# Optimization experiments

Measured on AMD Instinct MI355X. Metric: run time of the kernel, lower is better.

## Reference

```python
import jax, jax.numpy as jnp
import numpy as np

N = 100000
E = 1600000
H = 2          # attention heads
C = 64         # hidden_dim (per-head out channels)
VOCAB = 501    # attr_dims[0] + 1
NUM_GRAPHS = 512
NEG_SLOPE = 0.2


def gat_conv(h_in, src, dst, W, a_src, a_dst, bias):
    # h_in: [N, Fin]; W: [Fin, H*C]; a_src/a_dst: [H, C]; bias: [H*C]
    h = (h_in @ W).reshape(N, H, C)                      # [N,H,C]
    alpha_s = jnp.sum(h * a_src[None], axis=-1)          # [N,H]
    alpha_d = jnp.sum(h * a_dst[None], axis=-1)          # [N,H]
    e = jax.nn.leaky_relu(alpha_s[src] + alpha_d[dst], NEG_SLOPE)  # [Etot,H]
    # segment softmax over incoming edges of each dst node
    m = jax.ops.segment_max(e, dst, num_segments=N)      # [N,H]
    ex = jnp.exp(e - m[dst])
    s = jax.ops.segment_sum(ex, dst, num_segments=N)     # [N,H]
    alpha = ex / (s[dst] + 1e-16)                        # [Etot,H]
    out = jax.ops.segment_sum(h[src] * alpha[:, :, None], dst, num_segments=N)
    return out.reshape(N, H * C) + bias


def layer_norm(x, g, b):
    mu = jnp.mean(x, axis=-1, keepdims=True)
    var = jnp.var(x, axis=-1, keepdims=True)
    return (x - mu) / jnp.sqrt(var + 1e-5) * g + b


def setup_inputs() -> dict:
    key = jax.random.key(0)
    ks = jax.random.split(key, 16)
    x = jax.random.randint(ks[0], (N, 1), 0, 500, dtype=jnp.int64)
    edge_index = jax.random.randint(ks[1], (2, E), 0, N, dtype=jnp.int64)
    batch_idx = jnp.sort(jax.random.randint(ks[2], (N,), 0, NUM_GRAPHS, dtype=jnp.int64))
    sc = 0.1
    return {
        "x": x, "edge_index": edge_index, "batch_idx": batch_idx,
        "emb": jax.random.normal(ks[3], (VOCAB, C), jnp.float32) * sc,
        "W1": jax.random.normal(ks[4], (C, H * C), jnp.float32) * sc,
        "a_src1": jax.random.normal(ks[5], (H, C), jnp.float32) * sc,
        "a_dst1": jax.random.normal(ks[6], (H, C), jnp.float32) * sc,
        "b1": jnp.zeros((H * C,), jnp.float32),
        "ln_g": jnp.ones((H * C,), jnp.float32),
        "ln_b": jnp.zeros((H * C,), jnp.float32),
        "W2": jax.random.normal(ks[7], (H * C, H * C), jnp.float32) * sc,
        "a_src2": jax.random.normal(ks[8], (H, C), jnp.float32) * sc,
        "a_dst2": jax.random.normal(ks[9], (H, C), jnp.float32) * sc,
        "b2": jnp.zeros((H * C,), jnp.float32),
        "Wp": jax.random.normal(ks[10], (H * C, C), jnp.float32) * sc,
        "bp": jnp.zeros((C,), jnp.float32),
    }


def reference(x, edge_index, batch_idx, emb, W1, a_src1, a_dst1, b1, ln_g, ln_b, W2, a_src2, a_dst2, b2, Wp, bp):
    # add self-loops (PyG GATConv default add_self_loops=True)
    loops = jnp.arange(N, dtype=edge_index.dtype)
    src = jnp.concatenate([edge_index[0], loops])
    dst = jnp.concatenate([edge_index[1], loops])

    x_emb = emb[x[:, 0]]                                  # [N,C] (embedding + squeeze(1))
    h = gat_conv(x_emb, src, dst, W1, a_src1, a_dst1, b1)  # [N,2C]
    h = jax.nn.gelu(layer_norm(h, ln_g, ln_b), approximate=False)  # dropout off (eval)
    h = gat_conv(h, src, dst, W2, a_src2, a_dst2, b2)      # [N,2C]
    h = h @ Wp + bp                                        # [N,C]
    # global mean pool over graphs
    ssum = jax.ops.segment_sum(h, batch_idx, num_segments=NUM_GRAPHS)
    cnt = jax.ops.segment_sum(jnp.ones((N,), h.dtype), batch_idx, num_segments=NUM_GRAPHS)
    z = ssum / jnp.maximum(cnt, 1.0)[:, None]
    return h, z
```

## Files before the change

kernel.cpp:

```cpp
#include <hip/hip_runtime.h>
#include <hip/hip_bf16.h>
#include <math.h>

#define H2C 128
#define CDIM 64
#define CAP 48

typedef short s16x8 __attribute__((ext_vector_type(8)));
typedef unsigned short u16x8 __attribute__((ext_vector_type(8)));
typedef float f32x4 __attribute__((ext_vector_type(4)));

static __device__ __forceinline__ float wred64(float x) {
#pragma unroll
  for (int off = 32; off; off >>= 1) x += __shfl_xor(x, off, 64);
  return x;
}
static __device__ __forceinline__ ushort f2bfu(float x) {
  __hip_bfloat16 b = __float2bfloat16(x);
  return *reinterpret_cast<ushort*>(&b);
}
static __device__ __forceinline__ float bfu2f(ushort u) {
  unsigned int x = ((unsigned int)u) << 16;
  return __int_as_float((int)x);
}
static __device__ __forceinline__ float erf_fast(float x) {
  float ax = fabsf(x);
  float t = __fdividef(1.f, 1.f + 0.3275911f * ax);
  float y = t * (0.254829592f + t * (-0.284496736f +
            t * (1.421413741f + t * (-1.453152027f + t * 1.061405429f))));
  float e = 1.f - y * __expf(-ax * ax);
  return copysignf(e, x);
}

__global__ void k_embw(const float* __restrict__ emb, const float* __restrict__ W1,
                       const float* __restrict__ a_src, const float* __restrict__ a_dst,
                       float* __restrict__ embW, float* __restrict__ asv, float* __restrict__ adv)
{
  int v = blockIdx.x;
  int j = threadIdx.x;
  const float* er = emb + v * CDIM;
  float acc = 0.f;
#pragma unroll
  for (int k = 0; k < CDIM; ++k) acc += er[k] * W1[k * H2C + j];
  embW[v * H2C + j] = acc;
  float ps = wred64(acc * a_src[j]);
  float pd = wred64(acc * a_dst[j]);
  if ((j & 63) == 0) {
    int h = j >> 6;
    asv[v * 2 + h] = ps;
    adv[v * 2 + h] = pd;
  }
}

__global__ void k_w2prep(const float* __restrict__ W2,
                         const float* __restrict__ as2w, const float* __restrict__ ad2w,
                         ushort* __restrict__ w2bt, float* __restrict__ was, float* __restrict__ wad)
{
  int k = blockIdx.x;
  int c = threadIdx.x;
  float w = W2[k * H2C + c];
  w2bt[c * H2C + k] = f2bfu(w);
  int h = c >> 6;
  float s = wred64(w * as2w[c]);
  float d = wred64(w * ad2w[c]);
  if ((c & 63) == 0) { was[k * 2 + h] = s; wad[k * 2 + h] = d; }
}

__global__ void k_wpprep(const float* __restrict__ Wp, ushort* __restrict__ wpbt)
{
  int k = blockIdx.x;
  int c = threadIdx.x;
  wpbt[c * H2C + k] = f2bfu(Wp[k * CDIM + c]);
}

__global__ void __launch_bounds__(256)
k_scatter(const int* __restrict__ ei, const int* __restrict__ xv,
          int* __restrict__ count, unsigned* __restrict__ col4,
          int E, int N, int chunk)
{
  int xcd = blockIdx.x & 7;
  int ig  = blockIdx.x >> 3;
  int nb  = gridDim.x >> 3;
  int lo = xcd * chunk;
  int hi = lo + chunk; if (hi > N) hi = N;
  int stride = nb * 256;
  for (int e = ig * 256 + threadIdx.x; e < E; e += stride) {
    int d = ei[E + e];
    if (d < lo || d >= hi) continue;
    int s = ei[e];
    int slot = atomicAdd(&count[d], 1);
    if (slot < CAP)
      col4[(size_t)d * CAP + slot] = (unsigned)s | ((unsigned)xv[s] << 17);
  }
}

__global__ void __launch_bounds__(256)
k_gath1(const int* __restrict__ count, const unsigned* __restrict__ col4,
        const int* __restrict__ xv,
        const float2* __restrict__ asv, const float2* __restrict__ adv,
        const float* __restrict__ embW,
        const float* __restrict__ b1, const float* __restrict__ lng,
        const float* __restrict__ lnb,
        const float* __restrict__ was, const float* __restrict__ wad,
        ushort* __restrict__ g, float2* __restrict__ as2,
        float2* __restrict__ ad2, int N)
{
  int lane = threadIdx.x & 63;
  int wv = (blockIdx.x * blockDim.x + threadIdx.x) >> 6;
  int nw = (gridDim.x * blockDim.x) >> 6;
  int grp = lane >> 4, l16 = lane & 15;
  int headL = l16 >> 3;
  int cb = l16 * 8;
  float b1c[8], lngc[8], lnbc[8], was0[8], was1[8], wad0[8], wad1[8];
#pragma unroll
  for (int j = 0; j < 8; ++j) {
    b1c[j] = b1[cb + j]; lngc[j] = lng[cb + j]; lnbc[j] = lnb[cb + j];
    was0[j] = was[(cb + j) * 2]; was1[j] = was[(cb + j) * 2 + 1];
    wad0[j] = wad[(cb + j) * 2]; wad1[j] = wad[(cb + j) * 2 + 1];
  }
  for (int base = wv * 4; base < N; base += nw * 4) {
    int r = base + grp;
    bool valid = r < N;
    int cnt = 0, vd = 0;
    float adh = 0.f;
    if (valid) {
      cnt = count[r]; if (cnt > CAP) cnt = CAP;
      vd = xv[r];
      float2 ad = adv[vd];
      adh = headL ? ad.y : ad.x;
    }
    size_t rb = (size_t)r * CAP;
    float acc[8] = {0.f, 0.f, 0.f, 0.f, 0.f, 0.f, 0.f, 0.f};
    float s = 0.f;
    auto proc = [&](int vi) {
      float2 a_ = asv[vi];
      float e = (headL ? a_.y : a_.x) + adh; e = e >= 0.f ? e : 0.2f * e;
      float ex = __expf(e);
      s += ex;
      const float4* vp = (const float4*)&embW[(size_t)vi * H2C + cb];
      float4 va = vp[0], vb = vp[1];
      acc[0] += ex * va.x; acc[1] += ex * va.y;
      acc[2] += ex * va.z; acc[3] += ex * va.w;
      acc[4] += ex * vb.x; acc[5] += ex * vb.y;
      acc[6] += ex * vb.z; acc[7] += ex * vb.w;
    };
    proc(vd);
    int p = 0;
    for (; p + 4 <= cnt; p += 4) {
      uint4 q = *(const uint4*)&col4[rb + p];
      proc((int)(q.x >> 17)); proc((int)(q.y >> 17));
      proc((int)(q.z >> 17)); proc((int)(q.w >> 17));
    }
    for (; p < cnt; ++p) proc((int)(col4[rb + p] >> 17));
    float rr = __fdividef(1.f, s + 1e-16f);
    float x[8], sum = 0.f, ssq = 0.f;
#pragma unroll
    for (int j = 0; j < 8; ++j) {
      x[j] = acc[j] * rr + b1c[j];
      sum += x[j]; ssq += x[j] * x[j];
    }
#pragma unroll
    for (int off = 1; off < 16; off <<= 1) {
      sum += __shfl_xor(sum, off, 64);
      ssq += __shfl_xor(ssq, off, 64);
    }
    float mean = sum * (1.f / 128.f);
    float var  = ssq * (1.f / 128.f) - mean * mean;
    float rstd = rsqrtf(var + 1e-5f);
    float ps0 = 0.f, ps1 = 0.f, pd0 = 0.f, pd1 = 0.f;
    u16x8 gv;
#pragma unroll
    for (int j = 0; j < 8; ++j) {
      float t = (x[j] - mean) * rstd * lngc[j] + lnbc[j];
      t = 0.5f * t * (1.f + erf_fast(t * 0.70710678118654752f));
      gv[j] = f2bfu(t);
      ps0 += t * was0[j]; ps1 += t * was1[j];
      pd0 += t * wad0[j]; pd1 += t * wad1[j];
    }
#pragma unroll
    for (int off = 1; off < 16; off <<= 1) {
      ps0 += __shfl_xor(ps0, off, 64); ps1 += __shfl_xor(ps1, off, 64);
      pd0 += __shfl_xor(pd0, off, 64); pd1 += __shfl_xor(pd1, off, 64);
    }
    if (valid) {
      *(u16x8*)&g[(size_t)r * H2C + cb] = gv;
      if (l16 == 0) {
        as2[r] = make_float2(ps0, ps1);
        ad2[r] = make_float2(pd0, pd1);
      }
    }
  }
}

__global__ void __launch_bounds__(256)
k_gath2(const int* __restrict__ count, const unsigned* __restrict__ col4,
        const float2* __restrict__ as2, const float2* __restrict__ ad2,
        const ushort* __restrict__ h2b, const float* __restrict__ b2,
        ushort* __restrict__ g2, int N)
{
  int lane = threadIdx.x & 63;
  int wv = (blockIdx.x * blockDim.x + threadIdx.x) >> 6;
  int nw = (gridDim.x * blockDim.x) >> 6;
  int grp = lane >> 4, l16 = lane & 15;
  int headL = l16 >> 3;
  int cb = l16 * 8;
  float b2c[8];
#pragma unroll
  for (int j = 0; j < 8; ++j) b2c[j] = b2[cb + j];
  for (int base = wv * 4; base < N; base += nw * 4) {
    int r = base + grp;
    bool valid = r < N;
    int cnt = 0;
    float adh = 0.f;
    if (valid) {
      cnt = count[r]; if (cnt > CAP) cnt = CAP;
      float2 ad = ad2[r];
      adh = headL ? ad.y : ad.x;
    }
    size_t rb = (size_t)r * CAP;
    float acc[8] = {0.f, 0.f, 0.f, 0.f, 0.f, 0.f, 0.f, 0.f};
    float s = 0.f;
    auto proc = [&](int si) {
      float2 a_ = as2[si];
      float e = (headL ? a_.y : a_.x) + adh; e = e >= 0.f ? e : 0.2f * e;
      float ex = __expf(e);
      s += ex;
      u16x8 v = *(const u16x8*)&h2b[(size_t)si * H2C + cb];
#pragma unroll
      for (int j = 0; j < 8; ++j) acc[j] += ex * bfu2f(v[j]);
    };
    if (valid) proc(r);
    int p = 0;
    for (; p + 4 <= cnt; p += 4) {
      uint4 q = *(const uint4*)&col4[rb + p];
      proc((int)(q.x & 0x1FFFFu)); proc((int)(q.y & 0x1FFFFu));
      proc((int)(q.z & 0x1FFFFu)); proc((int)(q.w & 0x1FFFFu));
    }
    for (; p < cnt; ++p) proc((int)(col4[rb + p] & 0x1FFFFu));
    float rr = __fdividef(1.f, s + 1e-16f);
    u16x8 gv;
#pragma unroll
    for (int j = 0; j < 8; ++j) gv[j] = f2bfu(acc[j] * rr + b2c[j]);
    if (valid) *(u16x8*)&g2[(size_t)r * H2C + cb] = gv;
  }
}

__global__ void __launch_bounds__(256) k_gemm(const ushort* __restrict__ g,
                                              const ushort* __restrict__ w2bt,
                                              ushort* __restrict__ h2b, int N)
{
  __shared__ ushort As[H2C * H2C];
  __shared__ ushort Bs[H2C * H2C];
  int tid = threadIdx.x, lane = tid & 63, wv = tid >> 6;
  size_t rbase = (size_t)blockIdx.x * 128;

#pragma unroll
  for (int it = 0; it < 8; ++it) {
    int cb = (it * 4 + wv) * 64;
    int chunk = cb + lane;
    int row = chunk >> 4, kc = chunk & 15;
    int sc = (row << 4) | (kc ^ (row & 7));
    __builtin_amdgcn_global_load_lds(
        (const __attribute__((address_space(1))) void*)(g + rbase * H2C + (size_t)sc * 8),
        (__attribute__((address_space(3))) void*)(As + cb * 8), 16, 0, 0);
    __builtin_amdgcn_global_load_lds(
        (const __attribute__((address_space(1))) void*)(w2bt + (size_t)sc * 8),
        (__attribute__((address_space(3))) void*)(Bs + cb * 8), 16, 0, 0);
  }
  __syncthreads();

  f32x4 acc[2][8];
#pragma unroll
  for (int i = 0; i < 2; ++i)
#pragma unroll
    for (int j = 0; j < 8; ++j) acc[i][j] = (f32x4)0.f;

  int r15 = lane & 15, kg = lane >> 4;
#pragma unroll
  for (int ks = 0; ks < 4; ++ks) {
    int kc = ks * 4 + kg;
    s16x8 af[2], bfr[8];
#pragma unroll
    for (int mr = 0; mr < 2; ++mr) {
      int row = wv * 32 + mr * 16 + r15;
      af[mr] = *(const s16x8*)&As[row * H2C + (kc ^ (row & 7)) * 8];
    }
#pragma unroll
    for (int cf = 0; cf < 8; ++cf) {
      int row = cf * 16 + r15;
      bfr[cf] = *(const s16x8*)&Bs[row * H2C + (kc ^ (row & 7)) * 8];
    }
#pragma unroll
    for (int mr = 0; mr < 2; ++mr)
#pragma unroll
      for (int cf = 0; cf < 8; ++cf)
        acc[mr][cf] = __builtin_amdgcn_mfma_f32_16x16x32_bf16(af[mr], bfr[cf], acc[mr][cf], 0, 0, 0);
  }

#pragma unroll
  for (int mr = 0; mr < 2; ++mr) {
    int row0 = (int)rbase + wv * 32 + mr * 16 + kg * 4;
#pragma unroll
    for (int r = 0; r < 4; ++r) {
      int row = row0 + r;
      if (row < N) {
#pragma unroll
        for (int cf = 0; cf < 8; ++cf)
          h2b[(size_t)row * H2C + cf * 16 + r15] = f2bfu(acc[mr][cf][r]);
      }
    }
  }
}

__global__ void __launch_bounds__(256) k_gemmP(const ushort* __restrict__ g2,
                                               const ushort* __restrict__ wpbt,
                                               const float* __restrict__ bp,
                                               float* __restrict__ h3, int N)
{
  __shared__ ushort As[H2C * H2C];
  __shared__ ushort Bs[CDIM * H2C];
  int tid = threadIdx.x, lane = tid & 63, wv = tid >> 6;
  size_t rbase = (size_t)blockIdx.x * 128;

#pragma unroll
  for (int it = 0; it < 8; ++it) {
    int cb = (it * 4 + wv) * 64;
    int chunk = cb + lane;
    int row = chunk >> 4, kc = chunk & 15;
    int sc = (row << 4) | (kc ^ (row & 7));
    __builtin_amdgcn_global_load_lds(
        (const __attribute__((address_space(1))) void*)(g2 + rbase * H2C + (size_t)sc * 8),
        (__attribute__((address_space(3))) void*)(As + cb * 8), 16, 0, 0);
  }
#pragma unroll
  for (int it = 0; it < 4; ++it) {
    int cb = (it * 4 + wv) * 64;
    int chunk = cb + lane;
    int row = chunk >> 4, kc = chunk & 15;
    int sc = (row << 4) | (kc ^ (row & 7));
    __builtin_amdgcn_global_load_lds(
        (const __attribute__((address_space(1))) void*)(wpbt + (size_t)sc * 8),
        (__attribute__((address_space(3))) void*)(Bs + cb * 8), 16, 0, 0);
  }
  __syncthreads();

  f32x4 acc[2][4];
#pragma unroll
  for (int i = 0; i < 2; ++i)
#pragma unroll
    for (int j = 0; j < 4; ++j) acc[i][j] = (f32x4)0.f;

  int r15 = lane & 15, kg = lane >> 4;
#pragma unroll
  for (int ks = 0; ks < 4; ++ks) {
    int kc = ks * 4 + kg;
    s16x8 af[2], bfr[4];
#pragma unroll
    for (int mr = 0; mr < 2; ++mr) {
      int row = wv * 32 + mr * 16 + r15;
      af[mr] = *(const s16x8*)&As[row * H2C + (kc ^ (row & 7)) * 8];
    }
#pragma unroll
    for (int cf = 0; cf < 4; ++cf) {
      int row = cf * 16 + r15;
      bfr[cf] = *(const s16x8*)&Bs[row * H2C + (kc ^ (row & 7)) * 8];
    }
#pragma unroll
    for (int mr = 0; mr < 2; ++mr)
#pragma unroll
      for (int cf = 0; cf < 4; ++cf)
        acc[mr][cf] = __builtin_amdgcn_mfma_f32_16x16x32_bf16(af[mr], bfr[cf], acc[mr][cf], 0, 0, 0);
  }

#pragma unroll
  for (int mr = 0; mr < 2; ++mr) {
    int row0 = (int)rbase + wv * 32 + mr * 16 + kg * 4;
#pragma unroll
    for (int r = 0; r < 4; ++r) {
      int row = row0 + r;
      if (row < N) {
#pragma unroll
        for (int cf = 0; cf < 4; ++cf)
          h3[(size_t)row * CDIM + cf * 16 + r15] = acc[mr][cf][r] + bp[cf * 16 + r15];
      }
    }
  }
}

__global__ void __launch_bounds__(256)
k_pool(const float* __restrict__ h3, const int* __restrict__ bidx,
       float* __restrict__ z, int N)
{
  __shared__ float sh[4][64];
  int g = blockIdx.x;
  int lane = threadIdx.x & 63;
  int w = threadIdx.x >> 6;
  int lo = 0, hi = N;
  while (lo < hi) { int mid = (lo + hi) >> 1; if (bidx[mid] < g) lo = mid + 1; else hi = mid; }
  int s0 = lo;
  hi = N;
  while (lo < hi) { int mid = (lo + hi) >> 1; if (bidx[mid] < g + 1) lo = mid + 1; else hi = mid; }
  int s1 = lo;
  float sum = 0.f;
  for (int i = s0 + w; i < s1; i += 4) sum += h3[(size_t)i * CDIM + lane];
  sh[w][lane] = sum;
  __syncthreads();
  if (w == 0) {
    sum = sh[0][lane] + sh[1][lane] + sh[2][lane] + sh[3][lane];
    z[g * CDIM + lane] = sum / fmaxf((float)(s1 - s0), 1.f);
  }
}

extern "C" void kernel_launch(void* const* d_in, const int* in_sizes, int n_in,
                              void* d_out, int out_size, void* d_ws, size_t ws_size,
                              hipStream_t stream)
{
  const int*   xv   = (const int*)d_in[0];
  const int*   ei   = (const int*)d_in[1];
  const int*   bidx = (const int*)d_in[2];
  const float* emb  = (const float*)d_in[3];
  const float* W1   = (const float*)d_in[4];
  const float* as1  = (const float*)d_in[5];
  const float* ad1  = (const float*)d_in[6];
  const float* b1   = (const float*)d_in[7];
  const float* lng  = (const float*)d_in[8];
  const float* lnb  = (const float*)d_in[9];
  const float* W2   = (const float*)d_in[10];
  const float* as2w = (const float*)d_in[11];
  const float* ad2w = (const float*)d_in[12];
  const float* b2   = (const float*)d_in[13];
  const float* Wp   = (const float*)d_in[14];
  const float* bp   = (const float*)d_in[15];

  const int N   = in_sizes[2];
  const int E   = in_sizes[1] / 2;
  const int V   = in_sizes[3] / CDIM;
  const int NG  = (out_size - N * CDIM) / CDIM;
  const int NB  = (N + 127) / 128;
  const size_t NPAD = (size_t)NB * 128;

  size_t off = 0;
  auto alloc = [&](size_t bytes) -> void* {
    void* p = (char*)d_ws + off;
    off += (bytes + 255) & ~(size_t)255;
    return p;
  };
  float*  embW   = (float*)alloc((size_t)V * H2C * 4);
  float*  asv    = (float*)alloc((size_t)V * 2 * 4);
  float*  adv    = (float*)alloc((size_t)V * 2 * 4);
  ushort* w2bt   = (ushort*)alloc((size_t)H2C * H2C * 2);
  ushort* wpbt   = (ushort*)alloc((size_t)CDIM * H2C * 2);
  float*  was    = (float*)alloc((size_t)H2C * 2 * 4);
  float*  wad    = (float*)alloc((size_t)H2C * 2 * 4);
  ushort* g      = (ushort*)alloc(NPAD * H2C * 2);
  ushort* h2b    = (ushort*)alloc((size_t)N * H2C * 2);
  ushort* g2     = (ushort*)alloc(NPAD * H2C * 2);
  float2* as2    = (float2*)alloc((size_t)N * 8);
  float2* ad2    = (float2*)alloc((size_t)N * 8);
  int*    count  = (int*)alloc((size_t)N * 4);
  unsigned* col4 = (unsigned*)alloc((size_t)N * CAP * 4);
  (void)ws_size; (void)n_in;

  const int chunk8 = (N + 7) / 8;

  hipMemsetAsync(count, 0, (size_t)N * 4, stream);
  k_embw<<<V, 128, 0, stream>>>(emb, W1, as1, ad1, embW, asv, adv);
  k_w2prep<<<H2C, H2C, 0, stream>>>(W2, as2w, ad2w, w2bt, was, wad);
  k_wpprep<<<H2C, CDIM, 0, stream>>>(Wp, wpbt);
  k_scatter<<<2048, 256, 0, stream>>>(ei, xv, count, col4, E, N, chunk8);
  k_gath1<<<2048, 256, 0, stream>>>(count, col4, xv, (const float2*)asv,
                                    (const float2*)adv, embW, b1, lng, lnb,
                                    was, wad, g, as2, ad2, N);
  k_gemm<<<NB, 256, 0, stream>>>(g, w2bt, h2b, N);
  k_gath2<<<2048, 256, 0, stream>>>(count, col4, as2, ad2, h2b, b2, g2, N);
  float* outh = (float*)d_out;
  k_gemmP<<<NB, 256, 0, stream>>>(g2, wpbt, bp, outh, N);
  k_pool<<<NG, 256, 0, stream>>>(outh, bidx, outh + (size_t)N * CDIM, N);
}
```

Measured before the change: 278.9 us.

## Bin edges by destination chunk before per-XCD adjacency scatter

Replaces the scatter kernel, which had each XCD group scan the full edge list, with a two-pass scheme. The first pass bins edges by destination chunk using shared-memory counters and a few global atomics. The second pass has each XCD group process only its bin, in two half-range sweeps to keep atomic targets more cache-local. This removes the 8x redundant reads of edge indices, in exchange for an extra launch, an intermediate bin buffer, and a fixed bin capacity that may overflow on skewed destination distributions.

```diff
diff --git a/kernel.cpp b/kernel.cpp
--- a/kernel.cpp
+++ b/kernel.cpp
@@ -74,23 +74,59 @@
 }
 
 __global__ void __launch_bounds__(256)
-k_scatter(const int* __restrict__ ei, const int* __restrict__ xv,
-          int* __restrict__ count, unsigned* __restrict__ col4,
-          int E, int N, int chunk)
+k_binA(const int* __restrict__ ei, int* __restrict__ bincnt,
+       unsigned* __restrict__ bins, int E, int chunk, int binCap)
+{
+  __shared__ int lcnt[8];
+  __shared__ int lbase[8];
+  int t = threadIdx.x;
+  int stride = gridDim.x * 256;
+  for (int base = blockIdx.x * 256; base < E; base += stride) {
+    int e = base + t;
+    if (t < 8) lcnt[t] = 0;
+    __syncthreads();
+    int bin = 0, rank = 0; unsigned pay = 0; bool act = e < E;
+    if (act) {
+      int d = ei[E + e];
+      int s = ei[e];
+      bin = d / chunk;
+      pay = (unsigned)s | ((unsigned)(d - bin * chunk) << 17);
+      rank = atomicAdd(&lcnt[bin], 1);
+    }
+    __syncthreads();
+    if (t < 8) lbase[t] = lcnt[t] ? atomicAdd(&bincnt[t * 64], lcnt[t]) : 0;
+    __syncthreads();
+    if (act)
+      bins[(size_t)bin * binCap + lbase[bin] + rank] = pay;
+  }
+}
+
+__global__ void __launch_bounds__(256)
+k_binB(const unsigned* __restrict__ bins, const int* __restrict__ bincnt,
+       const int* __restrict__ xv, int* __restrict__ count,
+       unsigned* __restrict__ col4, int N, int chunk, int binCap)
 {
   int xcd = blockIdx.x & 7;
   int ig  = blockIdx.x >> 3;
   int nb  = gridDim.x >> 3;
   int lo = xcd * chunk;
-  int hi = lo + chunk; if (hi > N) hi = N;
+  int cnt = bincnt[xcd * 64];
+  const unsigned* bp = bins + (size_t)xcd * binCap;
   int stride = nb * 256;
-  for (int e = ig * 256 + threadIdx.x; e < E; e += stride) {
-    int d = ei[E + e];
-    if (d < lo || d >= hi) continue;
-    int s = ei[e];
-    int slot = atomicAdd(&count[d], 1);
-    if (slot < CAP)
-      col4[(size_t)d * CAP + slot] = (unsigned)s | ((unsigned)xv[s] << 17);
+  int halfc = chunk >> 1;
+  for (int half = 0; half < 2; ++half) {
+    int h0 = half * halfc;
+    int h1 = half ? chunk : halfc;
+    for (int i = ig * 256 + threadIdx.x; i < cnt; i += stride) {
+      unsigned p = bp[i];
+      int doff = (int)(p >> 17);
+      if (doff < h0 || doff >= h1) continue;
+      int s = (int)(p & 0x1FFFFu);
+      int d = lo + doff;
+      int slot = atomicAdd(&count[d], 1);
+      if (slot < CAP)
+        col4[(size_t)d * CAP + slot] = (unsigned)s | ((unsigned)xv[s] << 17);
+    }
   }
 }
 
@@ -438,6 +474,8 @@
   const int NG  = (out_size - N * CDIM) / CDIM;
   const int NB  = (N + 127) / 128;
   const size_t NPAD = (size_t)NB * 128;
+  const int chunk8 = (N + 7) / 8;
+  const int binCap = E / 8 + 65536;
 
   size_t off = 0;
   auto alloc = [&](size_t bytes) -> void* {
@@ -459,15 +497,17 @@
   float2* ad2    = (float2*)alloc((size_t)N * 8);
   int*    count  = (int*)alloc((size_t)N * 4);
   unsigned* col4 = (unsigned*)alloc((size_t)N * CAP * 4);
+  unsigned* bins = (unsigned*)alloc((size_t)8 * binCap * 4);
+  int*    bincnt = (int*)alloc(8 * 64 * 4);
   (void)ws_size; (void)n_in;
 
-  const int chunk8 = (N + 7) / 8;
-
   hipMemsetAsync(count, 0, (size_t)N * 4, stream);
+  hipMemsetAsync(bincnt, 0, 8 * 64 * 4, stream);
   k_embw<<<V, 128, 0, stream>>>(emb, W1, as1, ad1, embW, asv, adv);
   k_w2prep<<<H2C, H2C, 0, stream>>>(W2, as2w, ad2w, w2bt, was, wad);
   k_wpprep<<<H2C, CDIM, 0, stream>>>(Wp, wpbt);
-  k_scatter<<<2048, 256, 0, stream>>>(ei, xv, count, col4, E, N, chunk8);
+  k_binA<<<2048, 256, 0, stream>>>(ei, bincnt, bins, E, chunk8, binCap);
+  k_binB<<<2048, 256, 0, stream>>>(bins, bincnt, xv, count, col4, N, chunk8, binCap);
   k_gath1<<<2048, 256, 0, stream>>>(count, col4, xv, (const float2*)asv,
                                     (const float2*)adv, embW, b1, lng, lnb,
                                     was, wad, g, as2, ad2, N);
```

Result: slower. 363.2 us (+30.2%).
